# Kernel optimization log

Hardware: AMD Instinct MI355X
Metric: run time of the kernel (lower is better)

Reference implementation:

```python
import jax, jax.numpy as jnp
import numpy as np

EMBED_DIM = 512
NUM_HEADS = 8
HEAD_DIM = EMBED_DIM // NUM_HEADS


def setup_inputs() -> dict:
    key = jax.random.key(0)
    ks = jax.random.split(key, 9)
    s = 1.0 / np.sqrt(EMBED_DIM)
    x = jax.random.normal(ks[0], (2, 4096, EMBED_DIM), dtype=jnp.float32)
    return {
        "x": x,
        "Wq": jax.random.uniform(ks[1], (EMBED_DIM, EMBED_DIM), jnp.float32, -s, s),
        "bq": jax.random.uniform(ks[2], (EMBED_DIM,), jnp.float32, -s, s),
        "Wk": jax.random.uniform(ks[3], (EMBED_DIM, EMBED_DIM), jnp.float32, -s, s),
        "bk": jax.random.uniform(ks[4], (EMBED_DIM,), jnp.float32, -s, s),
        "Wv": jax.random.uniform(ks[5], (EMBED_DIM, EMBED_DIM), jnp.float32, -s, s),
        "bv": jax.random.uniform(ks[6], (EMBED_DIM,), jnp.float32, -s, s),
        "Wo": jax.random.uniform(ks[7], (EMBED_DIM, EMBED_DIM), jnp.float32, -s, s),
        "bo": jax.random.uniform(ks[8], (EMBED_DIM,), jnp.float32, -s, s),
    }


def reference(x, Wq, bq, Wk, bk, Wv, bv, Wo, bo):
    B, S, E = x.shape
    H, D = NUM_HEADS, HEAD_DIM
    # projections (torch Linear: x @ W.T + b)
    q = (x @ Wq.T + bq).reshape(B, S, H, D).transpose(0, 2, 1, 3)  # [B,H,S,D]
    k = (x @ Wk.T + bk).reshape(B, S, H, D).transpose(0, 2, 1, 3)
    v = (x @ Wv.T + bv).reshape(B, S, H, D).transpose(0, 2, 1, 3)
    scores = jnp.einsum("bhsd,bhtd->bhst", q, k) / np.sqrt(D)  # [B,H,S,S]
    attn = jax.nn.softmax(scores, axis=-1)
    out = jnp.einsum("bhst,bhtd->bhsd", attn, v)  # [B,H,S,D]
    out = out.transpose(0, 2, 1, 3).reshape(B, S, E)
    return out @ Wo.T + bo + x
```

## Files before the change

### kernel.cpp

```cpp
#include <hip/hip_runtime.h>
#include <hip/hip_bf16.h>


typedef __attribute__((ext_vector_type(8))) short short8;
typedef __attribute__((ext_vector_type(4))) short short4v;
typedef __attribute__((ext_vector_type(4))) float floatx4;
typedef __attribute__((ext_vector_type(2))) float floatx2;

#define SEQ 4096
#define EMB 512
#define NH 8
#define HD 64
#define MROWS 8192
#define SC2 0.18033688011112042f

__device__ inline unsigned short f2bf_rne(float f) {
    union { float f; unsigned int u; } c; c.f = f;
    unsigned int u = c.u;
    return (unsigned short)((u + 0x7FFFu + ((u >> 16) & 1u)) >> 16);
}

__device__ inline short8 load8f(const float* __restrict__ p) {
    float4 a = *(const float4*)p;
    float4 b = *(const float4*)(p + 4);
    short8 r;
    r[0] = (short)f2bf_rne(a.x); r[1] = (short)f2bf_rne(a.y);
    r[2] = (short)f2bf_rne(a.z); r[3] = (short)f2bf_rne(a.w);
    r[4] = (short)f2bf_rne(b.x); r[5] = (short)f2bf_rne(b.y);
    r[6] = (short)f2bf_rne(b.z); r[7] = (short)f2bf_rne(b.w);
    return r;
}

__device__ inline void gload_lds16(const unsigned short* g, unsigned short* l) {
    __builtin_amdgcn_global_load_lds(
        (__attribute__((address_space(1))) void*)(void*)g,
        (__attribute__((address_space(3))) void*)l,
        16, 0, 0);
}

__device__ inline unsigned int pk_bf2(float a, float b) {
    union { float f; unsigned int u; } ca, cb; ca.f = a; cb.f = b;
    return __builtin_amdgcn_perm(cb.u + 0x8000u, ca.u + 0x8000u, 0x07060302u);
}

__device__ inline unsigned int pk_bf2t(float a, float b) {
    union { float f; unsigned int u; } ca, cb; ca.f = a; cb.f = b;
    return __builtin_amdgcn_perm(cb.u, ca.u, 0x07060302u);
}

__global__ __launch_bounds__(256) void convert_kernel(
    const float* __restrict__ x, const float* __restrict__ Wq,
    const float* __restrict__ Wk, const float* __restrict__ Wv,
    const float* __restrict__ Wo, unsigned short* __restrict__ xb,
    unsigned short* __restrict__ wb)
{
    const size_t i8 = ((size_t)blockIdx.x * 256 + threadIdx.x) * 8;
    const float* src; unsigned short* dst;
    if (i8 < (size_t)MROWS * EMB) { src = x + i8; dst = xb + i8; }
    else {
        size_t j = i8 - (size_t)MROWS * EMB;
        int w = (int)(j >> 18); size_t off = j & 262143;
        src = (w == 0 ? Wq : w == 1 ? Wk : w == 2 ? Wv : Wo) + off;
        dst = wb + (size_t)w * 262144 + off;
    }
    *(short8*)dst = load8f(src);
}

__global__ __launch_bounds__(256) void qkv_kernel(
    const unsigned short* __restrict__ xb, const unsigned short* __restrict__ wb,
    const float* __restrict__ bq, const float* __restrict__ bk,
    const float* __restrict__ bv, unsigned short* __restrict__ Qo,
    unsigned short* __restrict__ Ko, unsigned short* __restrict__ VTo)
{
    __shared__ unsigned short smem[32768];

    const int tid = threadIdx.x, wave = tid >> 6, lane = tid & 63;
    const int quad = lane >> 4, l16 = lane & 15;
    const int wm = wave >> 1, wn = wave & 1;
    const int row0 = blockIdx.x * 128, col0 = blockIdx.y * 128;
    const int z = blockIdx.z;

    unsigned short* sA = smem;
    unsigned short* sB = smem + 16384;

    const unsigned short* A = xb + (size_t)row0 * EMB;
    const unsigned short* Bm = wb + (size_t)z * 262144 + (size_t)col0 * EMB;
    const float* bias = z == 0 ? bq : z == 1 ? bk : bv;
    unsigned short* out = z == 0 ? Qo : z == 1 ? Ko : VTo;

    auto stage = [&](int buf, int k0) {
#pragma unroll
        for (int it = 0; it < 4; ++it) {
            const int s = it * 256 + tid;
            const int row = s >> 3, cg = (s & 7) ^ (row & 7);
            const size_t go = (size_t)row * EMB + k0 + cg * 8;
            gload_lds16(A + go, &sA[buf * 8192 + (it * 256 + wave * 64) * 8]);
            gload_lds16(Bm + go, &sB[buf * 8192 + (it * 256 + wave * 64) * 8]);
        }
    };

    floatx4 acc[4][4];
#pragma unroll
    for (int i = 0; i < 4; ++i)
#pragma unroll
        for (int j = 0; j < 4; ++j) { floatx4 zz = {0.f,0.f,0.f,0.f}; acc[i][j] = zz; }

    stage(0, 0);
    int buf = 0;
    for (int k0 = 0; k0 < EMB; k0 += 64) {
        __syncthreads();
        if (k0 + 64 < EMB) stage(buf ^ 1, k0 + 64);
#pragma unroll
        for (int kk = 0; kk < 2; ++kk) {
            short8 a[4], b[4];
#pragma unroll
            for (int mi = 0; mi < 4; ++mi)
                a[mi] = *(const short8*)&sA[buf * 8192 + (wm * 64 + mi * 16 + l16) * 64 + (((kk * 4 + quad) ^ (l16 & 7)) << 3)];
#pragma unroll
            for (int ni = 0; ni < 4; ++ni)
                b[ni] = *(const short8*)&sB[buf * 8192 + (wn * 64 + ni * 16 + l16) * 64 + (((kk * 4 + quad) ^ (l16 & 7)) << 3)];
            if (z != 2) {
#pragma unroll
                for (int i = 0; i < 4; ++i)
#pragma unroll
                    for (int j = 0; j < 4; ++j)
                        acc[i][j] = __builtin_amdgcn_mfma_f32_16x16x32_bf16(b[i], a[j], acc[i][j], 0, 0, 0);
            } else {
#pragma unroll
                for (int i = 0; i < 4; ++i)
#pragma unroll
                    for (int j = 0; j < 4; ++j)
                        acc[i][j] = __builtin_amdgcn_mfma_f32_16x16x32_bf16(a[i], b[j], acc[i][j], 0, 0, 0);
            }
        }
        buf ^= 1;
    }

    __syncthreads();
    unsigned short* ct = smem;
    const float qs = (z == 0) ? SC2 : 1.0f;
    if (z != 2) {
#pragma unroll
        for (int i = 0; i < 4; ++i) {
            const int n0 = wn * 64 + i * 16 + quad * 4;
            const float4 fb = *(const float4*)&bias[col0 + n0];
#pragma unroll
            for (int j = 0; j < 4; ++j) {
                const int m = wm * 64 + j * 16 + l16;
                ushort4 pk;
                pk.x = f2bf_rne((acc[i][j][0] + fb.x) * qs);
                pk.y = f2bf_rne((acc[i][j][1] + fb.y) * qs);
                pk.z = f2bf_rne((acc[i][j][2] + fb.z) * qs);
                pk.w = f2bf_rne((acc[i][j][3] + fb.w) * qs);
                *(ushort4*)&ct[m * 132 + n0] = pk;
            }
        }
    } else {
#pragma unroll
        for (int j = 0; j < 4; ++j) {
            const int n = wn * 64 + j * 16 + l16;
            const float fb = bias[col0 + n];
#pragma unroll
            for (int i = 0; i < 4; ++i) {
                const int m0 = wm * 64 + i * 16 + quad * 4;
                ushort4 pk;
                pk.x = f2bf_rne(acc[i][j][0] + fb);
                pk.y = f2bf_rne(acc[i][j][1] + fb);
                pk.z = f2bf_rne(acc[i][j][2] + fb);
                pk.w = f2bf_rne(acc[i][j][3] + fb);
                *(ushort4*)&ct[n * 132 + m0] = pk;
            }
        }
    }
    __syncthreads();
#pragma unroll
    for (int it = 0; it < 8; ++it) {
        const int idx = it * 256 + tid;
        const int row = idx >> 4, chunk = idx & 15;
        short8 v = *(const short8*)&ct[row * 132 + chunk * 8];
        size_t addr;
        if (z != 2) {
            const int m_g = row0 + row;
            const int b = m_g >> 12, s = m_g & 4095;
            const int n_g = col0 + chunk * 8;
            const int h = n_g >> 6, d = n_g & 63;
            addr = ((size_t)((b * NH + h) * SEQ + s)) * HD + d;
        } else {
            const int n_g = col0 + row;
            const int h = n_g >> 6, d = n_g & 63;
            const int m_g = row0 + chunk * 8;
            const int b = m_g >> 12, s0 = m_g & 4095;
            addr = ((size_t)((b * NH + h) * HD + d)) * SEQ + s0;
        }
        *(short8*)&out[addr] = v;
    }
}

__global__ __launch_bounds__(256, 2) void attn_kernel(
    const unsigned short* __restrict__ Q, const unsigned short* __restrict__ K,
    const unsigned short* __restrict__ VT, unsigned short* __restrict__ Oout)
{
    __shared__ unsigned short smem[16384];
    __shared__ float sPS2[128];

    const int tid = threadIdx.x, wave = tid >> 6, lane = tid & 63;
    const int quad = lane >> 4, l16 = lane & 15;
    const int wq = wave >> 1, wt = wave & 1;
    const int bh = blockIdx.x, q0 = blockIdx.y * 128;
    const int xm = l16 & 7;

    const unsigned short* Qh = Q + (size_t)bh * SEQ * HD;
    const unsigned short* Kh = K + (size_t)bh * SEQ * HD;
    const unsigned short* Vh = VT + (size_t)bh * HD * SEQ;

    short8 qf[4][2];
#pragma unroll
    for (int mi = 0; mi < 4; ++mi)
#pragma unroll
        for (int kk = 0; kk < 2; ++kk)
            qf[mi][kk] = *(const short8*)(Qh + (size_t)(q0 + wq * 64 + mi * 16 + l16) * HD + kk * 32 + quad * 8);

    int kbase[2], kx0[2], kx1[2];
#pragma unroll
    for (int T = 0; T < 2; ++T) {
        const int R = wt * 32 + ((l16 >> 2) << 3) + (T << 2) + (l16 & 3);
        const int fR = (R & 7) ^ ((R >> 2) & 7);
        kbase[T] = R * 64;
        kx0[T] = (quad ^ fR) << 3;
        kx1[T] = ((4 + quad) ^ fR) << 3;
    }

    floatx4 oacc[4][4];
#pragma unroll
    for (int mi = 0; mi < 4; ++mi)
#pragma unroll
        for (int dt = 0; dt < 4; ++dt) { floatx4 zz = {0.f,0.f,0.f,0.f}; oacc[mi][dt] = zz; }
    floatx4 sacc[4];
#pragma unroll
    for (int mi = 0; mi < 4; ++mi) { floatx4 zz = {0.f,0.f,0.f,0.f}; sacc[mi] = zz; }
    const floatx4 z4 = {0.f, 0.f, 0.f, 0.f};
    const short ob = (short)0x3F80;
    const short8 ones8 = {ob, ob, ob, ob, ob, ob, ob, ob};

    auto stage = [&](int buf, int t0) {
#pragma unroll
        for (int psi = 0; psi < 2; ++psi) {
            const int r = psi * 32 + wave * 8 + (lane >> 3);
            const int j = lane & 7;
            const int cK = j ^ ((r & 7) ^ ((r >> 2) & 7));
            const int cV = j ^ (r & 7);
            gload_lds16(Kh + (size_t)(t0 + r) * HD + cK * 8,
                        &smem[buf * 4096 + psi * 2048 + wave * 512]);
            gload_lds16(Vh + (size_t)r * SEQ + t0 + cV * 8,
                        &smem[8192 + buf * 4096 + psi * 2048 + wave * 512]);
        }
    };

    stage(0, 0);
    int buf = 0;
    for (int t0 = 0; t0 < SEQ; t0 += 64) {
        __syncthreads();
        if (t0 + 64 < SEQ) stage(buf ^ 1, t0 + 64);

        const unsigned short* sKs  = &smem[buf * 4096];
        const unsigned short* sVTs = &smem[8192 + buf * 4096];

        short8 bK0[2], bK1[2];
#pragma unroll
        for (int T = 0; T < 2; ++T) {
            bK0[T] = *(const short8*)&sKs[kbase[T] + kx0[T]];
            bK1[T] = *(const short8*)&sKs[kbase[T] + kx1[T]];
        }
        short8 bv8[4];
#pragma unroll
        for (int dt = 0; dt < 4; ++dt)
            bv8[dt] = *(const short8*)&sVTs[(dt * 16 + l16) * 64 + (((wt * 4 + quad) ^ xm) << 3)];

#pragma unroll
        for (int mi = 0; mi < 4; ++mi) {
            floatx4 s0 = __builtin_amdgcn_mfma_f32_16x16x32_bf16(bK0[0], qf[mi][0], z4, 0, 0, 0);
            floatx4 s1 = __builtin_amdgcn_mfma_f32_16x16x32_bf16(bK0[1], qf[mi][0], z4, 0, 0, 0);
            s0 = __builtin_amdgcn_mfma_f32_16x16x32_bf16(bK1[0], qf[mi][1], s0, 0, 0, 0);
            s1 = __builtin_amdgcn_mfma_f32_16x16x32_bf16(bK1[1], qf[mi][1], s1, 0, 0, 0);

            const float e0 = __builtin_amdgcn_exp2f(s0[0]);
            const float e1 = __builtin_amdgcn_exp2f(s0[1]);
            const float e2 = __builtin_amdgcn_exp2f(s0[2]);
            const float e3 = __builtin_amdgcn_exp2f(s0[3]);
            const float e4 = __builtin_amdgcn_exp2f(s1[0]);
            const float e5 = __builtin_amdgcn_exp2f(s1[1]);
            const float e6 = __builtin_amdgcn_exp2f(s1[2]);
            const float e7 = __builtin_amdgcn_exp2f(s1[3]);
            union { uint4 u; short8 s; } cv;
            cv.u.x = pk_bf2t(e0, e1);
            cv.u.y = pk_bf2t(e2, e3);
            cv.u.z = pk_bf2t(e4, e5);
            cv.u.w = pk_bf2t(e6, e7);
            const short8 paf = cv.s;

            sacc[mi] = __builtin_amdgcn_mfma_f32_16x16x32_bf16(paf, ones8, sacc[mi], 0, 0, 0);
#pragma unroll
            for (int dt = 0; dt < 4; ++dt)
                oacc[mi][dt] = __builtin_amdgcn_mfma_f32_16x16x32_bf16(paf, bv8[dt], oacc[mi][dt], 0, 0, 0);
        }
        buf ^= 1;
    }

    __syncthreads();
    float* sRed = (float*)smem;
    if (wt == 1) {
#pragma unroll
        for (int mi = 0; mi < 4; ++mi) {
#pragma unroll
            for (int dt = 0; dt < 4; ++dt)
#pragma unroll
                for (int r = 0; r < 4; ++r)
                    sRed[wq * 4096 + (mi * 4 + dt) * 256 + (quad * 4 + r) * 16 + l16] = oacc[mi][dt][r];
            if (l16 == 0) {
#pragma unroll
                for (int r = 0; r < 4; ++r)
                    sPS2[wq * 64 + mi * 16 + quad * 4 + r] = sacc[mi][r];
            }
        }
    }
    __syncthreads();
    if (wt == 0) {
        const int b = bh >> 3, h = bh & 7;
#pragma unroll
        for (int mi = 0; mi < 4; ++mi) {
            float inv[4];
#pragma unroll
            for (int r = 0; r < 4; ++r)
                inv[r] = 1.0f / (sacc[mi][r] + sPS2[wq * 64 + mi * 16 + quad * 4 + r]);
#pragma unroll
            for (int dt = 0; dt < 4; ++dt)
#pragma unroll
                for (int r = 0; r < 4; ++r) {
                    const float o = oacc[mi][dt][r] +
                        sRed[wq * 4096 + (mi * 4 + dt) * 256 + (quad * 4 + r) * 16 + l16];
                    const int s = q0 + wq * 64 + mi * 16 + quad * 4 + r;
                    Oout[((size_t)b * SEQ + s) * EMB + h * HD + dt * 16 + l16] = f2bf_rne(o * inv[r]);
                }
        }
    }
}

__global__ __launch_bounds__(256) void outproj_kernel(
    const unsigned short* __restrict__ Ain, const unsigned short* __restrict__ wob,
    const float* __restrict__ bias, const float* __restrict__ X,
    float* __restrict__ out)
{
    __shared__ unsigned short sA[2][4096];
    __shared__ unsigned short sB[2][8192];

    const int tid = threadIdx.x, wave = tid >> 6, lane = tid & 63;
    const int quad = lane >> 4, l16 = lane & 15;
    const int wm = wave >> 1, wn = wave & 1;
    const int row0 = blockIdx.x * 64, col0 = blockIdx.y * 128;

    const unsigned short* A = Ain + (size_t)row0 * EMB;
    const unsigned short* Bm = wob + (size_t)col0 * EMB;

    auto stage = [&](int buf, int k0) {
#pragma unroll
        for (int it = 0; it < 2; ++it) {
            const int s = it * 256 + tid;
            const int row = s >> 3, cg = (s & 7) ^ (row & 7);
            gload_lds16(A + (size_t)row * EMB + k0 + cg * 8, &sA[buf][(it * 256 + wave * 64) * 8]);
        }
#pragma unroll
        for (int it = 0; it < 4; ++it) {
            const int s = it * 256 + tid;
            const int row = s >> 3, cg = (s & 7) ^ (row & 7);
            gload_lds16(Bm + (size_t)row * EMB + k0 + cg * 8, &sB[buf][(it * 256 + wave * 64) * 8]);
        }
    };

    floatx4 acc[2][4];
#pragma unroll
    for (int mi = 0; mi < 2; ++mi)
#pragma unroll
        for (int ni = 0; ni < 4; ++ni) { floatx4 zz = {0.f,0.f,0.f,0.f}; acc[mi][ni] = zz; }

    stage(0, 0);
    int buf = 0;
    for (int k0 = 0; k0 < EMB; k0 += 64) {
        __syncthreads();
        if (k0 + 64 < EMB) stage(buf ^ 1, k0 + 64);
#pragma unroll
        for (int kk = 0; kk < 2; ++kk) {
            short8 a[2], b[4];
#pragma unroll
            for (int mi = 0; mi < 2; ++mi)
                a[mi] = *(const short8*)&sA[buf][(wm * 32 + mi * 16 + l16) * 64 + (((kk * 4 + quad) ^ (l16 & 7)) << 3)];
#pragma unroll
            for (int ni = 0; ni < 4; ++ni)
                b[ni] = *(const short8*)&sB[buf][(wn * 64 + ni * 16 + l16) * 64 + (((kk * 4 + quad) ^ (l16 & 7)) << 3)];
#pragma unroll
            for (int mi = 0; mi < 2; ++mi)
#pragma unroll
                for (int ni = 0; ni < 4; ++ni)
                    acc[mi][ni] = __builtin_amdgcn_mfma_f32_16x16x32_bf16(a[mi], b[ni], acc[mi][ni], 0, 0, 0);
        }
        buf ^= 1;
    }

#pragma unroll
    for (int mi = 0; mi < 2; ++mi)
#pragma unroll
        for (int ni = 0; ni < 4; ++ni) {
            const int n = col0 + wn * 64 + ni * 16 + l16;
            const float bs = bias[n];
#pragma unroll
            for (int r = 0; r < 4; ++r) {
                const int m = row0 + wm * 32 + mi * 16 + quad * 4 + r;
                const size_t idx = (size_t)m * EMB + n;
                out[idx] = acc[mi][ni][r] + bs + X[idx];
            }
        }
}

extern "C" void kernel_launch(void* const* d_in, const int* in_sizes, int n_in,
                              void* d_out, int out_size, void* d_ws, size_t ws_size,
                              hipStream_t stream) {
    const float* x  = (const float*)d_in[0];
    const float* Wq = (const float*)d_in[1];
    const float* bq = (const float*)d_in[2];
    const float* Wk = (const float*)d_in[3];
    const float* bk = (const float*)d_in[4];
    const float* Wv = (const float*)d_in[5];
    const float* bv = (const float*)d_in[6];
    const float* Wo = (const float*)d_in[7];
    const float* bo = (const float*)d_in[8];
    float* out = (float*)d_out;

    const size_t SZ = (size_t)MROWS * EMB;
    unsigned short* wsXB = (unsigned short*)d_ws;
    unsigned short* wsWB = wsXB + SZ;
    unsigned short* wsQ  = wsWB + 4 * 262144;
    unsigned short* wsK  = wsQ + SZ;
    unsigned short* wsVT = wsK + SZ;

    convert_kernel<<<2560, 256, 0, stream>>>(x, Wq, Wk, Wv, Wo, wsXB, wsWB);
    qkv_kernel<<<dim3(MROWS / 128, EMB / 128, 3), 256, 0, stream>>>(
        wsXB, wsWB, bq, bk, bv, wsQ, wsK, wsVT);
    attn_kernel<<<dim3(2 * NH, SEQ / 128), 256, 0, stream>>>(wsQ, wsK, wsVT, wsXB);
    outproj_kernel<<<dim3(MROWS / 64, EMB / 128), 256, 0, stream>>>(
        wsXB, wsWB + 3 * 262144, bo, x, out);
}
```

Measured before the change: 191.1 us.

## Split attention keys across four waves per 64-query block, drop MFMA row-sum

Each attention block now covers 64 queries instead of 128, and all four waves share the same queries while each takes a different 32-key slice of a 128-key tile. The grid doubles to add parallelism, and occupancy is raised to three blocks per CU. Softmax row sums now come from VALU adds plus lane shuffles instead of an MFMA against a ones vector. The double-buffered K/V prefetch is dropped in favour of load, sync, then compute, which may expose memory latency. A three-way swizzled LDS reduction combines the partial outputs.

```diff
diff --git a/kernel.cpp b/kernel.cpp
--- a/kernel.cpp
+++ b/kernel.cpp
@@ -196,17 +196,16 @@
     }
 }
 
-__global__ __launch_bounds__(256, 2) void attn_kernel(
+__global__ __launch_bounds__(256, 3) void attn_kernel(
     const unsigned short* __restrict__ Q, const unsigned short* __restrict__ K,
     const unsigned short* __restrict__ VT, unsigned short* __restrict__ Oout)
 {
     __shared__ unsigned short smem[16384];
-    __shared__ float sPS2[128];
-
-    const int tid = threadIdx.x, wave = tid >> 6, lane = tid & 63;
+    __shared__ float sPS[3][64];
+
+    const int tid = threadIdx.x, wt = tid >> 6, lane = tid & 63;
     const int quad = lane >> 4, l16 = lane & 15;
-    const int wq = wave >> 1, wt = wave & 1;
-    const int bh = blockIdx.x, q0 = blockIdx.y * 128;
+    const int bh = blockIdx.x, q0 = blockIdx.y * 64;
     const int xm = l16 & 7;
 
     const unsigned short* Qh = Q + (size_t)bh * SEQ * HD;
@@ -218,7 +217,7 @@
     for (int mi = 0; mi < 4; ++mi)
 #pragma unroll
         for (int kk = 0; kk < 2; ++kk)
-            qf[mi][kk] = *(const short8*)(Qh + (size_t)(q0 + wq * 64 + mi * 16 + l16) * HD + kk * 32 + quad * 8);
+            qf[mi][kk] = *(const short8*)(Qh + (size_t)(q0 + mi * 16 + l16) * HD + kk * 32 + quad * 8);
 
     int kbase[2], kx0[2], kx1[2];
 #pragma unroll
@@ -235,46 +234,39 @@
     for (int mi = 0; mi < 4; ++mi)
 #pragma unroll
         for (int dt = 0; dt < 4; ++dt) { floatx4 zz = {0.f,0.f,0.f,0.f}; oacc[mi][dt] = zz; }
-    floatx4 sacc[4];
-#pragma unroll
-    for (int mi = 0; mi < 4; ++mi) { floatx4 zz = {0.f,0.f,0.f,0.f}; sacc[mi] = zz; }
+    floatx2 psum2[4] = {{0.f,0.f},{0.f,0.f},{0.f,0.f},{0.f,0.f}};
     const floatx4 z4 = {0.f, 0.f, 0.f, 0.f};
-    const short ob = (short)0x3F80;
-    const short8 ones8 = {ob, ob, ob, ob, ob, ob, ob, ob};
-
-    auto stage = [&](int buf, int t0) {
-#pragma unroll
-        for (int psi = 0; psi < 2; ++psi) {
-            const int r = psi * 32 + wave * 8 + (lane >> 3);
-            const int j = lane & 7;
-            const int cK = j ^ ((r & 7) ^ ((r >> 2) & 7));
-            const int cV = j ^ (r & 7);
-            gload_lds16(Kh + (size_t)(t0 + r) * HD + cK * 8,
-                        &smem[buf * 4096 + psi * 2048 + wave * 512]);
-            gload_lds16(Vh + (size_t)r * SEQ + t0 + cV * 8,
-                        &smem[8192 + buf * 4096 + psi * 2048 + wave * 512]);
+
+    auto stage = [&](int t0) {
+#pragma unroll
+        for (int it = 0; it < 4; ++it) {
+            const int s = it * 256 + tid;
+            const int rK = s >> 3, jK = s & 7;
+            const int cK = jK ^ ((rK & 7) ^ ((rK >> 2) & 7));
+            gload_lds16(Kh + (size_t)(t0 + rK) * HD + cK * 8,
+                        &smem[(it * 256 + wt * 64) * 8]);
+            const int rV = s >> 4, jV = s & 15;
+            const int cV = jV ^ (rV & 7);
+            gload_lds16(Vh + (size_t)rV * SEQ + t0 + cV * 8,
+                        &smem[8192 + (it * 256 + wt * 64) * 8]);
         }
     };
 
-    stage(0, 0);
-    int buf = 0;
-    for (int t0 = 0; t0 < SEQ; t0 += 64) {
+    for (int t0 = 0; t0 < SEQ; t0 += 128) {
         __syncthreads();
-        if (t0 + 64 < SEQ) stage(buf ^ 1, t0 + 64);
-
-        const unsigned short* sKs  = &smem[buf * 4096];
-        const unsigned short* sVTs = &smem[8192 + buf * 4096];
+        stage(t0);
+        __syncthreads();
 
         short8 bK0[2], bK1[2];
 #pragma unroll
         for (int T = 0; T < 2; ++T) {
-            bK0[T] = *(const short8*)&sKs[kbase[T] + kx0[T]];
-            bK1[T] = *(const short8*)&sKs[kbase[T] + kx1[T]];
+            bK0[T] = *(const short8*)&smem[kbase[T] + kx0[T]];
+            bK1[T] = *(const short8*)&smem[kbase[T] + kx1[T]];
         }
         short8 bv8[4];
 #pragma unroll
         for (int dt = 0; dt < 4; ++dt)
-            bv8[dt] = *(const short8*)&sVTs[(dt * 16 + l16) * 64 + (((wt * 4 + quad) ^ xm) << 3)];
+            bv8[dt] = *(const short8*)&smem[8192 + (dt * 16 + l16) * 128 + (((wt * 4 + quad) ^ xm) << 3)];
 
 #pragma unroll
         for (int mi = 0; mi < 4; ++mi) {
@@ -291,6 +283,8 @@
             const float e5 = __builtin_amdgcn_exp2f(s1[1]);
             const float e6 = __builtin_amdgcn_exp2f(s1[2]);
             const float e7 = __builtin_amdgcn_exp2f(s1[3]);
+            floatx2 pa = {e0, e1}, pb = {e2, e3}, pc = {e4, e5}, pd = {e6, e7};
+            psum2[mi] += (pa + pb) + (pc + pd);
             union { uint4 u; short8 s; } cv;
             cv.u.x = pk_bf2t(e0, e1);
             cv.u.y = pk_bf2t(e2, e3);
@@ -298,49 +292,87 @@
             cv.u.w = pk_bf2t(e6, e7);
             const short8 paf = cv.s;
 
-            sacc[mi] = __builtin_amdgcn_mfma_f32_16x16x32_bf16(paf, ones8, sacc[mi], 0, 0, 0);
 #pragma unroll
             for (int dt = 0; dt < 4; ++dt)
                 oacc[mi][dt] = __builtin_amdgcn_mfma_f32_16x16x32_bf16(paf, bv8[dt], oacc[mi][dt], 0, 0, 0);
         }
-        buf ^= 1;
+    }
+
+    float psum[4];
+#pragma unroll
+    for (int mi = 0; mi < 4; ++mi) {
+        psum[mi] = psum2[mi][0] + psum2[mi][1];
+        psum[mi] += __shfl_xor(psum[mi], 16);
+        psum[mi] += __shfl_xor(psum[mi], 32);
     }
 
     __syncthreads();
-    float* sRed = (float*)smem;
-    if (wt == 1) {
-#pragma unroll
-        for (int mi = 0; mi < 4; ++mi) {
+    float* sF = (float*)smem;
+    if (wt == 1 || wt == 3) {
+        float* reg = sF + (wt >> 1) * 4096;
+#pragma unroll
+        for (int mi = 0; mi < 4; ++mi)
 #pragma unroll
             for (int dt = 0; dt < 4; ++dt)
 #pragma unroll
-                for (int r = 0; r < 4; ++r)
-                    sRed[wq * 4096 + (mi * 4 + dt) * 256 + (quad * 4 + r) * 16 + l16] = oacc[mi][dt][r];
-            if (l16 == 0) {
-#pragma unroll
-                for (int r = 0; r < 4; ++r)
-                    sPS2[wq * 64 + mi * 16 + quad * 4 + r] = sacc[mi][r];
-            }
+                for (int r = 0; r < 4; ++r) {
+                    const int q = mi * 16 + quad * 4 + r;
+                    const int d = dt * 16 + l16;
+                    reg[q * 64 + (d ^ ((q & 7) << 3))] = oacc[mi][dt][r];
+                }
+    }
+    if (wt >= 1 && quad == 0) {
+#pragma unroll
+        for (int mi = 0; mi < 4; ++mi)
+            sPS[wt - 1][mi * 16 + l16] = psum[mi];
+    }
+    __syncthreads();
+    if (wt == 0 || wt == 2) {
+        float* reg = sF + (wt >> 1) * 4096;
+#pragma unroll
+        for (int mi = 0; mi < 4; ++mi)
+#pragma unroll
+            for (int dt = 0; dt < 4; ++dt)
+#pragma unroll
+                for (int r = 0; r < 4; ++r) {
+                    const int q = mi * 16 + quad * 4 + r;
+                    const int d = dt * 16 + l16;
+                    oacc[mi][dt][r] += reg[q * 64 + (d ^ ((q & 7) << 3))];
+                }
+        if (wt == 2) {
+#pragma unroll
+            for (int mi = 0; mi < 4; ++mi)
+#pragma unroll
+                for (int dt = 0; dt < 4; ++dt)
+#pragma unroll
+                    for (int r = 0; r < 4; ++r) {
+                        const int q = mi * 16 + quad * 4 + r;
+                        const int d = dt * 16 + l16;
+                        reg[q * 64 + (d ^ ((q & 7) << 3))] = oacc[mi][dt][r];
+                    }
         }
     }
     __syncthreads();
     if (wt == 0) {
+        float* reg = sF + 4096;
         const int b = bh >> 3, h = bh & 7;
 #pragma unroll
         for (int mi = 0; mi < 4; ++mi) {
-            float inv[4];
-#pragma unroll
-            for (int r = 0; r < 4; ++r)
-                inv[r] = 1.0f / (sacc[mi][r] + sPS2[wq * 64 + mi * 16 + quad * 4 + r]);
-#pragma unroll
-            for (int dt = 0; dt < 4; ++dt)
-#pragma unroll
-                for (int r = 0; r < 4; ++r) {
-                    const float o = oacc[mi][dt][r] +
-                        sRed[wq * 4096 + (mi * 4 + dt) * 256 + (quad * 4 + r) * 16 + l16];
-                    const int s = q0 + wq * 64 + mi * 16 + quad * 4 + r;
-                    Oout[((size_t)b * SEQ + s) * EMB + h * HD + dt * 16 + l16] = f2bf_rne(o * inv[r]);
+            const int ql = mi * 16 + l16;
+            const float pT = psum[mi] + sPS[0][ql] + sPS[1][ql] + sPS[2][ql];
+#pragma unroll
+            for (int r = 0; r < 4; ++r) {
+                const float inv = 1.0f / __shfl(pT, quad * 4 + r);
+                const int s = q0 + mi * 16 + quad * 4 + r;
+                const int q = mi * 16 + quad * 4 + r;
+                const size_t base = ((size_t)b * SEQ + s) * EMB + h * HD;
+#pragma unroll
+                for (int dt = 0; dt < 4; ++dt) {
+                    const int d = dt * 16 + l16;
+                    const float o = oacc[mi][dt][r] + reg[q * 64 + (d ^ ((q & 7) << 3))];
+                    Oout[base + d] = f2bf_rne(o * inv);
                 }
+            }
         }
     }
 }
@@ -444,7 +476,7 @@
     convert_kernel<<<2560, 256, 0, stream>>>(x, Wq, Wk, Wv, Wo, wsXB, wsWB);
     qkv_kernel<<<dim3(MROWS / 128, EMB / 128, 3), 256, 0, stream>>>(
         wsXB, wsWB, bq, bk, bv, wsQ, wsK, wsVT);
-    attn_kernel<<<dim3(2 * NH, SEQ / 128), 256, 0, stream>>>(wsQ, wsK, wsVT, wsXB);
+    attn_kernel<<<dim3(2 * NH, SEQ / 64), 256, 0, stream>>>(wsQ, wsK, wsVT, wsXB);
     outproj_kernel<<<dim3(MROWS / 64, EMB / 128), 256, 0, stream>>>(
         wsXB, wsWB + 3 * 262144, bo, x, out);
 }
```

Result: slower. 212.5 us (+11.2%).

## Halve attention query tile to 64 rows and batch score MFMAs for occupancy

Applied to the files above, without the earlier changes.

Each attention block now handles 64 query rows instead of 128, so the grid doubles to 1024 blocks and the launch bound asks for 4 blocks per CU. Per-wave accumulators shrink from 4 to 2 row tiles, cutting register pressure. The score MFMAs are regrouped so all QK products are issued before the exp2/pack step, giving more independent work between dependent instructions. The cost is that K/V tiles are loaded from global memory twice as often overall, since each staged tile now serves half as many queries.

```diff
diff --git a/kernel.cpp b/kernel.cpp
--- a/kernel.cpp
+++ b/kernel.cpp
@@ -196,29 +196,29 @@
     }
 }
 
-__global__ __launch_bounds__(256, 2) void attn_kernel(
+__global__ __launch_bounds__(256, 4) void attn_kernel(
     const unsigned short* __restrict__ Q, const unsigned short* __restrict__ K,
     const unsigned short* __restrict__ VT, unsigned short* __restrict__ Oout)
 {
     __shared__ unsigned short smem[16384];
-    __shared__ float sPS2[128];
+    __shared__ float sPS[128];
 
     const int tid = threadIdx.x, wave = tid >> 6, lane = tid & 63;
     const int quad = lane >> 4, l16 = lane & 15;
     const int wq = wave >> 1, wt = wave & 1;
-    const int bh = blockIdx.x, q0 = blockIdx.y * 128;
+    const int bh = blockIdx.x, q0 = blockIdx.y * 64;
     const int xm = l16 & 7;
 
     const unsigned short* Qh = Q + (size_t)bh * SEQ * HD;
     const unsigned short* Kh = K + (size_t)bh * SEQ * HD;
     const unsigned short* Vh = VT + (size_t)bh * HD * SEQ;
 
-    short8 qf[4][2];
-#pragma unroll
-    for (int mi = 0; mi < 4; ++mi)
+    short8 qf[2][2];
+#pragma unroll
+    for (int mi = 0; mi < 2; ++mi)
 #pragma unroll
         for (int kk = 0; kk < 2; ++kk)
-            qf[mi][kk] = *(const short8*)(Qh + (size_t)(q0 + wq * 64 + mi * 16 + l16) * HD + kk * 32 + quad * 8);
+            qf[mi][kk] = *(const short8*)(Qh + (size_t)(q0 + wq * 32 + mi * 16 + l16) * HD + kk * 32 + quad * 8);
 
     int kbase[2], kx0[2], kx1[2];
 #pragma unroll
@@ -230,14 +230,14 @@
         kx1[T] = ((4 + quad) ^ fR) << 3;
     }
 
-    floatx4 oacc[4][4];
-#pragma unroll
-    for (int mi = 0; mi < 4; ++mi)
+    floatx4 oacc[2][4];
+#pragma unroll
+    for (int mi = 0; mi < 2; ++mi)
 #pragma unroll
         for (int dt = 0; dt < 4; ++dt) { floatx4 zz = {0.f,0.f,0.f,0.f}; oacc[mi][dt] = zz; }
-    floatx4 sacc[4];
-#pragma unroll
-    for (int mi = 0; mi < 4; ++mi) { floatx4 zz = {0.f,0.f,0.f,0.f}; sacc[mi] = zz; }
+    floatx4 sacc[2];
+#pragma unroll
+    for (int mi = 0; mi < 2; ++mi) { floatx4 zz = {0.f,0.f,0.f,0.f}; sacc[mi] = zz; }
     const floatx4 z4 = {0.f, 0.f, 0.f, 0.f};
     const short ob = (short)0x3F80;
     const short8 ones8 = {ob, ob, ob, ob, ob, ob, ob, ob};
@@ -276,32 +276,43 @@
         for (int dt = 0; dt < 4; ++dt)
             bv8[dt] = *(const short8*)&sVTs[(dt * 16 + l16) * 64 + (((wt * 4 + quad) ^ xm) << 3)];
 
-#pragma unroll
-        for (int mi = 0; mi < 4; ++mi) {
-            floatx4 s0 = __builtin_amdgcn_mfma_f32_16x16x32_bf16(bK0[0], qf[mi][0], z4, 0, 0, 0);
-            floatx4 s1 = __builtin_amdgcn_mfma_f32_16x16x32_bf16(bK0[1], qf[mi][0], z4, 0, 0, 0);
-            s0 = __builtin_amdgcn_mfma_f32_16x16x32_bf16(bK1[0], qf[mi][1], s0, 0, 0, 0);
-            s1 = __builtin_amdgcn_mfma_f32_16x16x32_bf16(bK1[1], qf[mi][1], s1, 0, 0, 0);
-
-            const float e0 = __builtin_amdgcn_exp2f(s0[0]);
-            const float e1 = __builtin_amdgcn_exp2f(s0[1]);
-            const float e2 = __builtin_amdgcn_exp2f(s0[2]);
-            const float e3 = __builtin_amdgcn_exp2f(s0[3]);
-            const float e4 = __builtin_amdgcn_exp2f(s1[0]);
-            const float e5 = __builtin_amdgcn_exp2f(s1[1]);
-            const float e6 = __builtin_amdgcn_exp2f(s1[2]);
-            const float e7 = __builtin_amdgcn_exp2f(s1[3]);
+        floatx4 stf[2][2];
+#pragma unroll
+        for (int mi = 0; mi < 2; ++mi)
+#pragma unroll
+            for (int T = 0; T < 2; ++T)
+                stf[mi][T] = __builtin_amdgcn_mfma_f32_16x16x32_bf16(bK0[T], qf[mi][0], z4, 0, 0, 0);
+#pragma unroll
+        for (int mi = 0; mi < 2; ++mi)
+#pragma unroll
+            for (int T = 0; T < 2; ++T)
+                stf[mi][T] = __builtin_amdgcn_mfma_f32_16x16x32_bf16(bK1[T], qf[mi][1], stf[mi][T], 0, 0, 0);
+
+        short8 paf[2];
+#pragma unroll
+        for (int mi = 0; mi < 2; ++mi) {
+            const float e0 = __builtin_amdgcn_exp2f(stf[mi][0][0]);
+            const float e1 = __builtin_amdgcn_exp2f(stf[mi][0][1]);
+            const float e2 = __builtin_amdgcn_exp2f(stf[mi][0][2]);
+            const float e3 = __builtin_amdgcn_exp2f(stf[mi][0][3]);
+            const float e4 = __builtin_amdgcn_exp2f(stf[mi][1][0]);
+            const float e5 = __builtin_amdgcn_exp2f(stf[mi][1][1]);
+            const float e6 = __builtin_amdgcn_exp2f(stf[mi][1][2]);
+            const float e7 = __builtin_amdgcn_exp2f(stf[mi][1][3]);
             union { uint4 u; short8 s; } cv;
             cv.u.x = pk_bf2t(e0, e1);
             cv.u.y = pk_bf2t(e2, e3);
             cv.u.z = pk_bf2t(e4, e5);
             cv.u.w = pk_bf2t(e6, e7);
-            const short8 paf = cv.s;
-
-            sacc[mi] = __builtin_amdgcn_mfma_f32_16x16x32_bf16(paf, ones8, sacc[mi], 0, 0, 0);
+            paf[mi] = cv.s;
+        }
+
+#pragma unroll
+        for (int mi = 0; mi < 2; ++mi) {
+            sacc[mi] = __builtin_amdgcn_mfma_f32_16x16x32_bf16(paf[mi], ones8, sacc[mi], 0, 0, 0);
 #pragma unroll
             for (int dt = 0; dt < 4; ++dt)
-                oacc[mi][dt] = __builtin_amdgcn_mfma_f32_16x16x32_bf16(paf, bv8[dt], oacc[mi][dt], 0, 0, 0);
+                oacc[mi][dt] = __builtin_amdgcn_mfma_f32_16x16x32_bf16(paf[mi], bv8[dt], oacc[mi][dt], 0, 0, 0);
         }
         buf ^= 1;
     }
@@ -310,16 +321,16 @@
     float* sRed = (float*)smem;
     if (wt == 1) {
 #pragma unroll
-        for (int mi = 0; mi < 4; ++mi) {
+        for (int mi = 0; mi < 2; ++mi) {
 #pragma unroll
             for (int dt = 0; dt < 4; ++dt)
 #pragma unroll
                 for (int r = 0; r < 4; ++r)
-                    sRed[wq * 4096 + (mi * 4 + dt) * 256 + (quad * 4 + r) * 16 + l16] = oacc[mi][dt][r];
+                    sRed[wq * 2048 + (mi * 4 + dt) * 256 + (quad * 4 + r) * 16 + l16] = oacc[mi][dt][r];
             if (l16 == 0) {
 #pragma unroll
                 for (int r = 0; r < 4; ++r)
-                    sPS2[wq * 64 + mi * 16 + quad * 4 + r] = sacc[mi][r];
+                    sPS[wq * 64 + mi * 16 + quad * 4 + r] = sacc[mi][r];
             }
         }
     }
@@ -327,18 +338,18 @@
     if (wt == 0) {
         const int b = bh >> 3, h = bh & 7;
 #pragma unroll
-        for (int mi = 0; mi < 4; ++mi) {
+        for (int mi = 0; mi < 2; ++mi) {
             float inv[4];
 #pragma unroll
             for (int r = 0; r < 4; ++r)
-                inv[r] = 1.0f / (sacc[mi][r] + sPS2[wq * 64 + mi * 16 + quad * 4 + r]);
+                inv[r] = 1.0f / (sacc[mi][r] + sPS[wq * 64 + mi * 16 + quad * 4 + r]);
 #pragma unroll
             for (int dt = 0; dt < 4; ++dt)
 #pragma unroll
                 for (int r = 0; r < 4; ++r) {
                     const float o = oacc[mi][dt][r] +
-                        sRed[wq * 4096 + (mi * 4 + dt) * 256 + (quad * 4 + r) * 16 + l16];
-                    const int s = q0 + wq * 64 + mi * 16 + quad * 4 + r;
+                        sRed[wq * 2048 + (mi * 4 + dt) * 256 + (quad * 4 + r) * 16 + l16];
+                    const int s = q0 + wq * 32 + mi * 16 + quad * 4 + r;
                     Oout[((size_t)b * SEQ + s) * EMB + h * HD + dt * 16 + l16] = f2bf_rne(o * inv[r]);
                 }
         }
@@ -444,7 +455,7 @@
     convert_kernel<<<2560, 256, 0, stream>>>(x, Wq, Wk, Wv, Wo, wsXB, wsWB);
     qkv_kernel<<<dim3(MROWS / 128, EMB / 128, 3), 256, 0, stream>>>(
         wsXB, wsWB, bq, bk, bv, wsQ, wsK, wsVT);
-    attn_kernel<<<dim3(2 * NH, SEQ / 128), 256, 0, stream>>>(wsQ, wsK, wsVT, wsXB);
+    attn_kernel<<<dim3(2 * NH, SEQ / 64), 256, 0, stream>>>(wsQ, wsK, wsVT, wsXB);
     outproj_kernel<<<dim3(MROWS / 64, EMB / 128), 256, 0, stream>>>(
         wsXB, wsWB + 3 * 262144, bo, x, out);
 }
```

Measured after the change: 196.2 us. +2.6%, slower.
